# Kernel tuning notes

Measured on AMD Instinct MI355X. Metric: run time of the kernel, lower is better.

Reference implementation:

```python
import jax, jax.numpy as jnp
import numpy as np

NA, NT = 50000, 100000          # address / transaction node counts
FA, FT = 128, 64                # raw feature dims per node type
HID, OUT, HEADS, NCLS = 128, 64, 8, 2
E1, E2 = 500000, 250000         # cross-type / same-type edge counts
NEG_SLOPE = 0.2
LN_EPS = 1e-5


def _edge_att(xs, xd, src, dst, a_s, a_d, n_dst):
    # xs: [Ns,H,D] projected src feats, xd: [Nd,H,D] projected dst feats
    alpha_s = (xs * a_s).sum(-1)                     # [Ns,H]
    alpha_d = (xd * a_d).sum(-1)                     # [Nd,H]
    alpha = alpha_s[src] + alpha_d[dst]              # [E,H]
    alpha = jnp.where(alpha > 0, alpha, NEG_SLOPE * alpha)  # leaky_relu(0.2)
    # segment softmax over incoming edges of each dst node
    m = jax.lax.stop_gradient(jax.ops.segment_max(alpha, dst, num_segments=n_dst))
    m = jnp.where(jnp.isfinite(m), m, 0.0)
    ex = jnp.exp(alpha - m[dst])
    denom = jax.ops.segment_sum(ex, dst, num_segments=n_dst)
    w = ex / jnp.maximum(denom[dst], 1e-16)          # [E,H]
    msg = xs[src] * w[:, :, None]                    # [E,H,D]
    out = jax.ops.segment_sum(msg, dst, num_segments=n_dst)
    return jax.nn.relu(out.reshape(n_dst, -1))       # [Nd, H*D] (HANConv relu per edge type)


def _group(outs, q, kW, kb):
    # semantic-level attention over metapaths; outs: [K,N,F]
    score = (jnp.tanh(outs @ kW + kb).mean(axis=1) * q).sum(-1)  # [K]
    attn = jax.nn.softmax(score)
    return jnp.einsum('k,knf->nf', attn, outs)


def _layer_norm(x, g, b):
    mu = x.mean(-1, keepdims=True)
    var = ((x - mu) ** 2).mean(-1, keepdims=True)
    return (x - mu) / jnp.sqrt(var + LN_EPS) * g + b


def _han_conv(xa, xt, edges, Wa, ba, Wt, bt, atts, q, kW, kb):
    C = Wa.shape[1]
    D = C // HEADS
    za = (xa @ Wa + ba).reshape(-1, HEADS, D)
    zt = (xt @ Wt + bt).reshape(-1, HEADS, D)
    (eat_s, eat_d), (eta_s, eta_d), (eaa_s, eaa_d), (ett_s, ett_d) = edges
    (as_at, ad_at), (as_ta, ad_ta), (as_aa, ad_aa), (as_tt, ad_tt) = atts
    o_at = _edge_att(za, zt, eat_s, eat_d, as_at, ad_at, zt.shape[0])  # -> transaction
    o_ta = _edge_att(zt, za, eta_s, eta_d, as_ta, ad_ta, za.shape[0])  # -> address
    o_aa = _edge_att(za, za, eaa_s, eaa_d, as_aa, ad_aa, za.shape[0])  # -> address
    o_tt = _edge_att(zt, zt, ett_s, ett_d, as_tt, ad_tt, zt.shape[0])  # -> transaction
    new_a = _group(jnp.stack([o_ta, o_aa]), q, kW, kb)
    new_t = _group(jnp.stack([o_at, o_tt]), q, kW, kb)
    return new_a, new_t


def _forward(x_address, x_transaction,
             W_a1, b_a1, W_t1, b_t1,
             as_at1, ad_at1, as_ta1, ad_ta1, as_aa1, ad_aa1, as_tt1, ad_tt1,
             k1_W, k1_b, q1,
             W_a2, b_a2, W_t2, b_t2,
             as_at2, ad_at2, as_ta2, ad_ta2, as_aa2, ad_aa2, as_tt2, ad_tt2,
             k2_W, k2_b, q2,
             ln1_g, ln1_b, ln2_g, ln2_b, lin_W, lin_b, edges):
    atts1 = ((as_at1, ad_at1), (as_ta1, ad_ta1), (as_aa1, ad_aa1), (as_tt1, ad_tt1))
    atts2 = ((as_at2, ad_at2), (as_ta2, ad_ta2), (as_aa2, ad_aa2), (as_tt2, ad_tt2))
    xa, xt = _han_conv(x_address, x_transaction, edges, W_a1, b_a1, W_t1, b_t1, atts1, q1, k1_W, k1_b)
    xa = jax.nn.relu(_layer_norm(xa, ln1_g, ln1_b))
    xt = jax.nn.relu(_layer_norm(xt, ln1_g, ln1_b))
    # dropout is identity in eval mode
    xa, xt = _han_conv(xa, xt, edges, W_a2, b_a2, W_t2, b_t2, atts2, q2, k2_W, k2_b)
    xa = jax.nn.relu(_layer_norm(xa, ln2_g, ln2_b))
    return xa @ lin_W + lin_b                          # [NA, NCLS]


def setup_inputs() -> dict:
    key = jax.random.key(0)
    ks = jax.random.split(key, 40)
    D1, D2 = HID // HEADS, OUT // HEADS
    def n(i, shape, s=0.1):
        return jax.random.normal(ks[i], shape, jnp.float32) * s
    inp = {
        'x_address': jax.random.normal(ks[0], (NA, FA), jnp.float32),
        'x_transaction': jax.random.normal(ks[1], (NT, FT), jnp.float32),
        'eat_src': jax.random.randint(ks[2], (E1,), 0, NA),
        'eat_dst': jax.random.randint(ks[3], (E1,), 0, NT),
        'eta_src': jax.random.randint(ks[4], (E1,), 0, NT),
        'eta_dst': jax.random.randint(ks[5], (E1,), 0, NA),
        'eaa_src': jax.random.randint(ks[6], (E2,), 0, NA),
        'eaa_dst': jax.random.randint(ks[7], (E2,), 0, NA),
        'ett_src': jax.random.randint(ks[8], (E2,), 0, NT),
        'ett_dst': jax.random.randint(ks[9], (E2,), 0, NT),
        'W_a1': n(10, (FA, HID)), 'b_a1': jnp.zeros((HID,), jnp.float32),
        'W_t1': n(11, (FT, HID)), 'b_t1': jnp.zeros((HID,), jnp.float32),
        'as_at1': n(12, (HEADS, D1)), 'ad_at1': n(13, (HEADS, D1)),
        'as_ta1': n(14, (HEADS, D1)), 'ad_ta1': n(15, (HEADS, D1)),
        'as_aa1': n(16, (HEADS, D1)), 'ad_aa1': n(17, (HEADS, D1)),
        'as_tt1': n(18, (HEADS, D1)), 'ad_tt1': n(19, (HEADS, D1)),
        'k1_W': n(20, (HID, HID)), 'k1_b': jnp.zeros((HID,), jnp.float32), 'q1': n(21, (HID,)),
        'W_a2': n(22, (HID, OUT)), 'b_a2': jnp.zeros((OUT,), jnp.float32),
        'W_t2': n(23, (HID, OUT)), 'b_t2': jnp.zeros((OUT,), jnp.float32),
        'as_at2': n(24, (HEADS, D2)), 'ad_at2': n(25, (HEADS, D2)),
        'as_ta2': n(26, (HEADS, D2)), 'ad_ta2': n(27, (HEADS, D2)),
        'as_aa2': n(28, (HEADS, D2)), 'ad_aa2': n(29, (HEADS, D2)),
        'as_tt2': n(30, (HEADS, D2)), 'ad_tt2': n(31, (HEADS, D2)),
        'k2_W': n(32, (OUT, OUT)), 'k2_b': jnp.zeros((OUT,), jnp.float32), 'q2': n(33, (OUT,)),
        'ln1_g': jnp.ones((HID,), jnp.float32), 'ln1_b': jnp.zeros((HID,), jnp.float32),
        'ln2_g': jnp.ones((OUT,), jnp.float32), 'ln2_b': jnp.zeros((OUT,), jnp.float32),
        'lin_W': n(34, (OUT, NCLS)), 'lin_b': jnp.zeros((NCLS,), jnp.float32),
    }
    return inp


def reference(x_address, x_transaction,
              eat_src, eat_dst, eta_src, eta_dst, eaa_src, eaa_dst, ett_src, ett_dst,
              W_a1, b_a1, W_t1, b_t1,
              as_at1, ad_at1, as_ta1, ad_ta1, as_aa1, ad_aa1, as_tt1, ad_tt1,
              k1_W, k1_b, q1,
              W_a2, b_a2, W_t2, b_t2,
              as_at2, ad_at2, as_ta2, ad_ta2, as_aa2, ad_aa2, as_tt2, ad_tt2,
              k2_W, k2_b, q2,
              ln1_g, ln1_b, ln2_g, ln2_b, lin_W, lin_b):
    edges = ((eat_src, eat_dst), (eta_src, eta_dst), (eaa_src, eaa_dst), (ett_src, ett_dst))
    return _forward(x_address, x_transaction,
                    W_a1, b_a1, W_t1, b_t1,
                    as_at1, ad_at1, as_ta1, ad_ta1, as_aa1, ad_aa1, as_tt1, ad_tt1,
                    k1_W, k1_b, q1,
                    W_a2, b_a2, W_t2, b_t2,
                    as_at2, ad_at2, as_ta2, ad_ta2, as_aa2, ad_aa2, as_tt2, ad_tt2,
                    k2_W, k2_b, q2,
                    ln1_g, ln1_b, ln2_g, ln2_b, lin_W, lin_b, edges)
```

## Files before the change

### kernel.cpp

```cpp
#include <hip/hip_runtime.h>
#include <cstdint>
#include <cstddef>
#include <type_traits>

#define NA 50000
#define NT 100000
#define FA 128
#define FT 64
#define HID 128
#define OUTF 64
#define HEADS 8
#define E1 500000
#define E2 250000
#define NTOT (2*NT + 2*NA)
#define ETOT (2*E1 + 2*E2)
#define NSH 8

typedef __attribute__((ext_vector_type(8))) short short8;
typedef __attribute__((ext_vector_type(4))) float f32x4;

static __device__ __forceinline__ ushort f2b(float f) {
  unsigned int u = __float_as_uint(f);
  return (ushort)((u + 0x7fffu + ((u >> 16) & 1u)) >> 16);
}
static __device__ __forceinline__ float b2f(ushort b) {
  return __uint_as_float(((unsigned int)b) << 16);
}
static __device__ __forceinline__ float u2f_lo(unsigned int u) {
  return __uint_as_float(u << 16);
}
static __device__ __forceinline__ float u2f_hi(unsigned int u) {
  return __uint_as_float(u & 0xffff0000u);
}

template<int KK, typename AT>
__device__ __forceinline__ void gemm_fullk(
    const AT* __restrict__ A, const float* __restrict__ W,
    int N, int M, int row0, int col0,
    ushort* __restrict__ Als, ushort* __restrict__ Bls, f32x4* acc)
{
  constexpr int LP = KK + 8;
  int t = threadIdx.x;
  int w = t >> 6, lane = t & 63;
  int l15 = lane & 15, l4 = lane >> 4;
  {
    int arow = t >> 2, ac0 = (t & 3) * (KK / 4);
    bool aok = (row0 + arow) < N;
    const AT* Ap = A + (size_t)(row0 + arow) * KK + ac0;
#pragma unroll
    for (int j = 0; j < KK / 32; j++) {
      union { ushort u[8]; uint4 v; } pa;
      if (aok) {
        if constexpr (std::is_same<AT, float>::value) {
          float4 a0 = *reinterpret_cast<const float4*>(Ap + j*8);
          float4 a1 = *reinterpret_cast<const float4*>(Ap + j*8 + 4);
          pa.u[0]=f2b(a0.x); pa.u[1]=f2b(a0.y); pa.u[2]=f2b(a0.z); pa.u[3]=f2b(a0.w);
          pa.u[4]=f2b(a1.x); pa.u[5]=f2b(a1.y); pa.u[6]=f2b(a1.z); pa.u[7]=f2b(a1.w);
        } else {
          pa.v = *reinterpret_cast<const uint4*>(Ap + j*8);
        }
      } else {
        pa.v = make_uint4(0,0,0,0);
      }
      *reinterpret_cast<uint4*>(&Als[arow * LP + ac0 + j*8]) = pa.v;
    }
  }
  {
    int col = t & 63, kb = t >> 6;
    const float* Wp = W + (size_t)(col0 + col);
#pragma unroll
    for (int j = 0; j < KK / 32; j++) {
      int k0 = kb * (KK / 4) + j * 8;
      union { ushort u[8]; uint4 v; } pb;
#pragma unroll
      for (int i = 0; i < 8; i++)
        pb.u[i] = f2b(Wp[(size_t)(k0 + i) * M]);
      *reinterpret_cast<uint4*>(&Bls[col * LP + k0]) = pb.v;
    }
  }
  __syncthreads();
#pragma unroll
  for (int ks = 0; ks < KK / 32; ks++) {
    short8 af = *reinterpret_cast<const short8*>(
        &Als[(16*w + l15) * LP + ks*32 + l4*8]);
#pragma unroll
    for (int n = 0; n < 4; n++) {
      short8 bf = *reinterpret_cast<const short8*>(
          &Bls[(16*n + l15) * LP + ks*32 + l4*8]);
      acc[n] = __builtin_amdgcn_mfma_f32_16x16x32_bf16(af, bf, acc[n], 0, 0, 0);
    }
  }
}

template<int NV, int DD, int KK, typename AT>
__global__ __launch_bounds__(256) void zgemm_k(
    const AT* __restrict__ A, const float* __restrict__ W,
    const float* __restrict__ bias,
    const float* __restrict__ v0, const float* __restrict__ v1,
    const float* __restrict__ v2, const float* __restrict__ v3,
    float* __restrict__ o0, float* __restrict__ o1,
    float* __restrict__ o2, float* __restrict__ o3,
    ushort* __restrict__ Cb, int N, int M)
{
  __shared__ __align__(16) ushort Als[64 * (KK + 8)];
  __shared__ __align__(16) ushort Bls[64 * (KK + 8)];
  int t = threadIdx.x;
  int row0 = blockIdx.x * 64, col0 = blockIdx.y * 64;
  int w = t >> 6, lane = t & 63;
  int l15 = lane & 15, l4 = lane >> 4;
  f32x4 acc[4] = {{0.f,0.f,0.f,0.f},{0.f,0.f,0.f,0.f},
                  {0.f,0.f,0.f,0.f},{0.f,0.f,0.f,0.f}};
  gemm_fullk<KK, AT>(A, W, N, M, row0, col0, Als, Bls, acc);

  float vals[4][4];
#pragma unroll
  for (int n = 0; n < 4; n++) {
    int col = col0 + 16*n + l15;
    float bv = bias[col];
#pragma unroll
    for (int r = 0; r < 4; r++) {
      int row = row0 + 16*w + l4*4 + r;
      float v = acc[n][r] + bv;
      vals[n][r] = v;
      if (row < N) Cb[(size_t)row * M + col] = f2b(v);
    }
  }
#pragma unroll
  for (int n = 0; n < 4; n++) {
    int head = (DD == 16) ? (blockIdx.y*4 + n) : (n*2 + (l15 >> 3));
    int vi = head * DD + (l15 & (DD - 1));
    float w0 = v0[vi];
    float w1 = (NV > 1) ? v1[vi] : 0.f;
    float w2 = (NV > 2) ? v2[vi] : 0.f;
    float w3 = (NV > 3) ? v3[vi] : 0.f;
#pragma unroll
    for (int r = 0; r < 4; r++) {
      int row = row0 + 16*w + l4*4 + r;
      float zv = vals[n][r];
      float a0 = zv * w0, a1 = zv * w1, a2 = zv * w2, a3 = zv * w3;
#pragma unroll
      for (int o = 1; o < DD; o <<= 1) {
        a0 += __shfl_xor(a0, o);
        if (NV > 1) a1 += __shfl_xor(a1, o);
        if (NV > 2) a2 += __shfl_xor(a2, o);
        if (NV > 3) a3 += __shfl_xor(a3, o);
      }
      if ((l15 & (DD - 1)) == 0 && row < N) {
        o0[(size_t)row * 8 + head] = a0;
        if (NV > 1) o1[(size_t)row * 8 + head] = a1;
        if (NV > 2) o2[(size_t)row * 8 + head] = a2;
        if (NV > 3) o3[(size_t)row * 8 + head] = a3;
      }
    }
  }
}

template<int KK>
__global__ __launch_bounds__(256) void score_k(
    const ushort* __restrict__ A0, const ushort* __restrict__ A1,
    const ushort* __restrict__ A2, const ushort* __restrict__ A3,
    const float* __restrict__ W, const float* __restrict__ bias,
    const float* __restrict__ qv, float* __restrict__ scp,
    int4 cum, int4 Ns, int4 Gs, int M)
{
  __shared__ __align__(16) ushort Als[64 * (KK + 8)];
  __shared__ __align__(16) ushort Bls[64 * (KK + 8)];
  __shared__ float red[4];
  int b = blockIdx.x;
  int tsk, base, G, N; const ushort* A;
  if      (b < cum.x) { tsk=0; base=0;     G=Gs.x; N=Ns.x; A=A0; }
  else if (b < cum.y) { tsk=1; base=cum.x; G=Gs.y; N=Ns.y; A=A1; }
  else if (b < cum.z) { tsk=2; base=cum.y; G=Gs.z; N=Ns.z; A=A2; }
  else                { tsk=3; base=cum.z; G=Gs.w; N=Ns.w; A=A3; }
  int local = b - base;
  int row0 = (local % G) * 64, col0 = (local / G) * 64;
  int t = threadIdx.x;
  int w = t >> 6, lane = t & 63;
  int l15 = lane & 15, l4 = lane >> 4;
  f32x4 acc[4] = {{0.f,0.f,0.f,0.f},{0.f,0.f,0.f,0.f},
                  {0.f,0.f,0.f,0.f},{0.f,0.f,0.f,0.f}};
  gemm_fullk<KK, ushort>(A, W, N, M, row0, col0, Als, Bls, acc);

  float local_s = 0.f;
#pragma unroll
  for (int n = 0; n < 4; n++) {
    int col = col0 + 16*n + l15;
    float bv = bias[col], qq = qv[col];
#pragma unroll
    for (int r = 0; r < 4; r++) {
      int row = row0 + 16*w + l4*4 + r;
      if (row < N) local_s += tanhf(acc[n][r] + bv) * qq;
    }
  }
#pragma unroll
  for (int o = 32; o > 0; o >>= 1) local_s += __shfl_xor(local_s, o);
  if (lane == 0) red[w] = local_s;
  __syncthreads();
  if (t == 0) atomicAdd(&scp[tsk], red[0] + red[1] + red[2] + red[3]);
}

__global__ void hist4_sh(const int* __restrict__ d0, const int* __restrict__ d1,
    const int* __restrict__ d2, const int* __restrict__ d3,
    int* __restrict__ cnt8, float* __restrict__ scp)
{
  if (blockIdx.x == 0 && threadIdx.x < 8) scp[threadIdx.x] = 0.f;
  int e = blockIdx.x * 256 + threadIdx.x;
  int sh = blockIdx.x & (NSH - 1);
  int d;
  if      (e < E1)          d = d0[e];
  else if (e < 2*E1)        d = d1[e - E1] + NT;
  else if (e < 2*E1 + E2)   d = d2[e - 2*E1] + NT + NA;
  else if (e < ETOT)        d = d3[e - 2*E1 - E2] + NT + 2*NA;
  else return;
  atomicAdd(&cnt8[sh * NTOT + d], 1);
}

__global__ void scatter_sh(const int* __restrict__ s0, const int* __restrict__ d0,
    const int* __restrict__ s1, const int* __restrict__ d1,
    const int* __restrict__ s2, const int* __restrict__ d2,
    const int* __restrict__ s3, const int* __restrict__ d3,
    int* __restrict__ cur8, int* __restrict__ ssh)
{
  int e = blockIdx.x * 256 + threadIdx.x;
  int sh = blockIdx.x & (NSH - 1);
  int d, s;
  if      (e < E1)          { d = d0[e];                           s = s0[e]; }
  else if (e < 2*E1)        { d = d1[e - E1] + NT;                 s = s1[e - E1]; }
  else if (e < 2*E1 + E2)   { d = d2[e - 2*E1] + NT + NA;          s = s2[e - 2*E1]; }
  else if (e < ETOT)        { d = d3[e - 2*E1 - E2] + NT + 2*NA;   s = s3[e - 2*E1 - E2]; }
  else return;
  int p = atomicAdd(&cur8[sh * NTOT + d], 1);
  ssh[p] = s;
}

__global__ void sumsh_k(const int* __restrict__ cnt8, int* __restrict__ cnt)
{
  int g = blockIdx.x * 256 + threadIdx.x;
  if (g >= NTOT) return;
  int s = 0;
#pragma unroll
  for (int k = 0; k < NSH; k++) s += cnt8[k * NTOT + g];
  cnt[g] = s;
}

__global__ void compact_k(const int* __restrict__ rp8, const int* __restrict__ rp,
    const int* __restrict__ ssh, int* __restrict__ ssrc)
{
  int g = blockIdx.x * 256 + threadIdx.x;
  if (g >= NTOT) return;
  int w = rp[g];
#pragma unroll
  for (int s = 0; s < NSH; s++) {
    int b0 = rp8[s * NTOT + g], b1 = rp8[s * NTOT + g + 1];
    for (int e = b0; e < b1; e++) ssrc[w++] = ssh[e];
  }
}

__global__ __launch_bounds__(256) void scan_blk(const int* __restrict__ in,
    int* __restrict__ rp1, int* __restrict__ bsum, int n)
{
  __shared__ int sh[256];
  int base = blockIdx.x * 2048;
  int t = threadIdx.x;
  int v[8]; int s = 0;
#pragma unroll
  for (int k = 0; k < 8; k++) {
    int i = base + t * 8 + k;
    v[k] = (i < n) ? in[i] : 0; s += v[k];
  }
  sh[t] = s; __syncthreads();
  for (int o = 1; o < 256; o <<= 1) {
    int x = (t >= o) ? sh[t - o] : 0;
    __syncthreads(); sh[t] += x; __syncthreads();
  }
  int run = (t == 0) ? 0 : sh[t - 1];
  if (t == 255 && bsum) bsum[blockIdx.x] = sh[255];
#pragma unroll
  for (int k = 0; k < 8; k++) {
    int i = base + t * 8 + k;
    run += v[k];
    if (i < n) rp1[i] = run;
  }
}

__global__ void scan_add2(int* __restrict__ rp, int* __restrict__ cur,
    const int* __restrict__ bsA, int n)
{
  int i = blockIdx.x * blockDim.x + threadIdx.x;
  if (i == 0) { rp[0] = 0; cur[0] = 0; }
  if (i < n) {
    int blk = i >> 11;
    int base = blk ? bsA[blk - 1] : 0;
    int v = rp[i + 1] + base;
    rp[i + 1] = v;
    if (i + 1 < n) cur[i + 1] = v;
  }
}

__global__ void scan_add(int* __restrict__ rp, const int* __restrict__ bsA, int n)
{
  int i = blockIdx.x * blockDim.x + threadIdx.x;
  if (i == 0) rp[0] = 0;
  if (i < n) {
    int blk = i >> 11;
    int base = blk ? bsA[blk - 1] : 0;
    rp[i + 1] += base;
  }
}

struct AggTask {
  int g0, Nd;
  const float* als; const float* ald;
  const ushort* z;  ushort* out;
};

template<int F>
__global__ __launch_bounds__(256) void agg_multi(const int* __restrict__ rp,
    const int* __restrict__ ssrc, AggTask T0, AggTask T1, AggTask T2, AggTask T3,
    int c1, int c2, int c3)
{
  constexpr int LPN = (F == 128) ? 16 : 8;
  constexpr int NPW = 64 / LPN;
  int b = blockIdx.x;
  AggTask T; int lb;
  if      (b < c1) { T = T0; lb = b; }
  else if (b < c2) { T = T1; lb = b - c1; }
  else if (b < c3) { T = T2; lb = b - c2; }
  else             { T = T3; lb = b - c3; }
  int wv = threadIdx.x >> 6, lane = threadIdx.x & 63;
  int grp = lane / LPN, lg = lane % LPN;
  int n = (lb * 4 + wv) * NPW + grp;
  if (n >= T.Nd) return;
  int g = T.g0 + n;
  int start = rp[g], end = rp[g + 1];
  int hh = (F == 128) ? (lg >> 1) : lg;
  float ad_h = T.ald[(size_t)n * 8 + hh];

  float den = 0.f;
  float acc[8] = {};
  for (int e = start; e < end; e++) {
    int sn = ssrc[e];
    uint4 zv = *reinterpret_cast<const uint4*>(T.z + (size_t)sn * F + lg * 8);
    float a = T.als[(size_t)sn * 8 + hh] + ad_h;
    a = a > 0.f ? a : 0.2f * a;
    float p = __expf(fminf(a, 30.f));
    den += p;
    acc[0] = fmaf(p, u2f_lo(zv.x), acc[0]);
    acc[1] = fmaf(p, u2f_hi(zv.x), acc[1]);
    acc[2] = fmaf(p, u2f_lo(zv.y), acc[2]);
    acc[3] = fmaf(p, u2f_hi(zv.y), acc[3]);
    acc[4] = fmaf(p, u2f_lo(zv.z), acc[4]);
    acc[5] = fmaf(p, u2f_hi(zv.z), acc[5]);
    acc[6] = fmaf(p, u2f_lo(zv.w), acc[6]);
    acc[7] = fmaf(p, u2f_hi(zv.w), acc[7]);
  }
  float inv = 1.f / fmaxf(den, 1e-16f);
  unsigned int pk[4];
#pragma unroll
  for (int k2 = 0; k2 < 4; k2++)
    pk[k2] = (unsigned int)f2b(fmaxf(acc[2*k2] * inv, 0.f))
           | ((unsigned int)f2b(fmaxf(acc[2*k2+1] * inv, 0.f)) << 16);
  *reinterpret_cast<uint4*>(T.out + (size_t)n * F + lg * 8)
      = make_uint4(pk[0], pk[1], pk[2], pk[3]);
}

__global__ __launch_bounds__(256) void combine2_k(
    const ushort* __restrict__ o00, const ushort* __restrict__ o01,
    const float* __restrict__ sc0, float invn0, ushort* __restrict__ out0, int N0,
    const ushort* __restrict__ o10, const ushort* __restrict__ o11,
    const float* __restrict__ sc1, float invn1, ushort* __restrict__ out1, int N1,
    const float* __restrict__ g, const float* __restrict__ bb)
{
  int c1 = (N0 + 3) / 4;
  int b = blockIdx.x;
  const ushort *o0, *o1; const float* sc; float invn; ushort* outp; int N, lb;
  if (b < c1) { o0=o00; o1=o01; sc=sc0; invn=invn0; outp=out0; N=N0; lb=b; }
  else        { o0=o10; o1=o11; sc=sc1; invn=invn1; outp=out1; N=N1; lb=b-c1; }
  int wv = threadIdx.x >> 6, lane = threadIdx.x & 63;
  int n = lb * 4 + wv;
  if (n >= N) return;
  float s0 = sc[0] * invn, s1 = sc[1] * invn;
  float mx = fmaxf(s0, s1);
  float e0 = __expf(s0 - mx), e1 = __expf(s1 - mx);
  float w0 = e0 / (e0 + e1), w1 = e1 / (e0 + e1);
  float x[2];
#pragma unroll
  for (int jj = 0; jj < 2; jj++) {
    int idx = lane + 64 * jj;
    x[jj] = w0 * b2f(o0[(size_t)n * 128 + idx]) + w1 * b2f(o1[(size_t)n * 128 + idx]);
  }
  float sum = x[0] + x[1];
#pragma unroll
  for (int o = 32; o > 0; o >>= 1) sum += __shfl_xor(sum, o);
  float mu = sum / 128.f;
  float vs = 0.f;
#pragma unroll
  for (int jj = 0; jj < 2; jj++) { float dd = x[jj] - mu; vs = fmaf(dd, dd, vs); }
#pragma unroll
  for (int o = 32; o > 0; o >>= 1) vs += __shfl_xor(vs, o);
  float rstd = rsqrtf(vs / 128.f + 1e-5f);
#pragma unroll
  for (int jj = 0; jj < 2; jj++) {
    int idx = lane + 64 * jj;
    float y = (x[jj] - mu) * rstd * g[idx] + bb[idx];
    outp[(size_t)n * 128 + idx] = f2b(fmaxf(y, 0.f));
  }
}

__global__ __launch_bounds__(256) void combine_final_k(
    const ushort* __restrict__ o0, const ushort* __restrict__ o1,
    const float* __restrict__ sc, float invn,
    const float* __restrict__ g, const float* __restrict__ bb,
    const float* __restrict__ lw, const float* __restrict__ lb,
    float* __restrict__ outp, int N)
{
  int wv = threadIdx.x >> 6, lane = threadIdx.x & 63;
  int n = blockIdx.x * 4 + wv;
  if (n >= N) return;
  float s0 = sc[0] * invn, s1 = sc[1] * invn;
  float mx = fmaxf(s0, s1);
  float e0 = __expf(s0 - mx), e1 = __expf(s1 - mx);
  float w0 = e0 / (e0 + e1), w1 = e1 / (e0 + e1);
  float x = w0 * b2f(o0[(size_t)n * 64 + lane]) + w1 * b2f(o1[(size_t)n * 64 + lane]);
  float sum = x;
#pragma unroll
  for (int o = 32; o > 0; o >>= 1) sum += __shfl_xor(sum, o);
  float mu = sum / 64.f;
  float dd = x - mu;
  float vs = dd * dd;
#pragma unroll
  for (int o = 32; o > 0; o >>= 1) vs += __shfl_xor(vs, o);
  float rstd = rsqrtf(vs / 64.f + 1e-5f);
  float y = fmaxf((x - mu) * rstd * g[lane] + bb[lane], 0.f);
  float p0 = y * lw[lane * 2 + 0];
  float p1 = y * lw[lane * 2 + 1];
#pragma unroll
  for (int o = 32; o > 0; o >>= 1) { p0 += __shfl_xor(p0, o); p1 += __shfl_xor(p1, o); }
  if (lane == 0) {
    outp[(size_t)n * 2 + 0] = p0 + lb[0];
    outp[(size_t)n * 2 + 1] = p1 + lb[1];
  }
}

extern "C" void kernel_launch(void* const* d_in, const int* in_sizes, int n_in,
                              void* d_out, int out_size, void* d_ws, size_t ws_size,
                              hipStream_t stream)
{
  (void)in_sizes; (void)n_in; (void)out_size;
  const float* x_a = (const float*)d_in[0];
  const float* x_t = (const float*)d_in[1];
  const int* eat_s = (const int*)d_in[2];
  const int* eat_d = (const int*)d_in[3];
  const int* eta_s = (const int*)d_in[4];
  const int* eta_d = (const int*)d_in[5];
  const int* eaa_s = (const int*)d_in[6];
  const int* eaa_d = (const int*)d_in[7];
  const int* ett_s = (const int*)d_in[8];
  const int* ett_d = (const int*)d_in[9];
  const float* W_a1 = (const float*)d_in[10]; const float* b_a1 = (const float*)d_in[11];
  const float* W_t1 = (const float*)d_in[12]; const float* b_t1 = (const float*)d_in[13];
  const float* as_at1 = (const float*)d_in[14]; const float* ad_at1 = (const float*)d_in[15];
  const float* as_ta1 = (const float*)d_in[16]; const float* ad_ta1 = (const float*)d_in[17];
  const float* as_aa1 = (const float*)d_in[18]; const float* ad_aa1 = (const float*)d_in[19];
  const float* as_tt1 = (const float*)d_in[20]; const float* ad_tt1 = (const float*)d_in[21];
  const float* k1_W = (const float*)d_in[22]; const float* k1_b = (const float*)d_in[23];
  const float* q1   = (const float*)d_in[24];
  const float* W_a2 = (const float*)d_in[25]; const float* b_a2 = (const float*)d_in[26];
  const float* W_t2 = (const float*)d_in[27]; const float* b_t2 = (const float*)d_in[28];
  const float* as_ta2 = (const float*)d_in[31]; const float* ad_ta2 = (const float*)d_in[32];
  const float* as_aa2 = (const float*)d_in[33]; const float* ad_aa2 = (const float*)d_in[34];
  const float* k2_W = (const float*)d_in[37]; const float* k2_b = (const float*)d_in[38];
  const float* q2   = (const float*)d_in[39];
  const float* ln1_g = (const float*)d_in[40]; const float* ln1_b = (const float*)d_in[41];
  const float* ln2_g = (const float*)d_in[42]; const float* ln2_b = (const float*)d_in[43];
  const float* lin_W = (const float*)d_in[44]; const float* lin_b = (const float*)d_in[45];

  char* ws = (char*)d_ws;
  size_t off = 0;
  auto alloc = [&](size_t bytes) {
    size_t o = off; off += (bytes + 255) & ~(size_t)255; return o;
  };
  size_t ZA1 = alloc((size_t)NA * HID * 2);
  size_t ZT1 = alloc((size_t)NT * HID * 2);
  size_t OTA = alloc((size_t)NA * HID * 2);
  size_t OAA = alloc((size_t)NA * HID * 2);
  size_t OAT = alloc((size_t)NT * HID * 2);
  size_t OTT = alloc((size_t)NT * HID * 2);
  size_t A_AS_AT = alloc((size_t)NA * 8 * 4);
  size_t A_AD_TA = alloc((size_t)NA * 8 * 4);
  size_t A_AS_AA = alloc((size_t)NA * 8 * 4);
  size_t A_AD_AA = alloc((size_t)NA * 8 * 4);
  size_t A_T_D_AT = alloc((size_t)NT * 8 * 4);
  size_t A_T_S_TA = alloc((size_t)NT * 8 * 4);
  size_t A_T_S_TT = alloc((size_t)NT * 8 * 4);
  size_t A_T_D_TT = alloc((size_t)NT * 8 * 4);
  size_t RP8  = alloc(((size_t)NSH * NTOT + 1) * 4);
  size_t CUR8 = alloc((size_t)NSH * NTOT * 4);
  size_t SSH  = alloc((size_t)ETOT * 4);
  size_t RP   = alloc((size_t)(NTOT + 1) * 4);
  size_t CNT  = alloc((size_t)NTOT * 4);
  size_t SS   = alloc((size_t)ETOT * 4);
  size_t BSM  = alloc(2048 * 4);
  size_t BSM2 = alloc(256 * 4);
  size_t SC   = alloc(256);
  if (off > ws_size) return;

  ushort* za1 = (ushort*)(ws + ZA1);
  ushort* zt1 = (ushort*)(ws + ZT1);
  ushort* ota = (ushort*)(ws + OTA);
  ushort* oaa = (ushort*)(ws + OAA);
  ushort* oat = (ushort*)(ws + OAT);
  ushort* ott = (ushort*)(ws + OTT);
  float* aASAT = (float*)(ws + A_AS_AT);
  float* aADTA = (float*)(ws + A_AD_TA);
  float* aASAA = (float*)(ws + A_AS_AA);
  float* aADAA = (float*)(ws + A_AD_AA);
  float* aTDAT = (float*)(ws + A_T_D_AT);
  float* aTSTA = (float*)(ws + A_T_S_TA);
  float* aTSTT = (float*)(ws + A_T_S_TT);
  float* aTDTT = (float*)(ws + A_T_D_TT);
  int* rp8  = (int*)(ws + RP8);
  int* cur8 = (int*)(ws + CUR8);
  int* ssh  = (int*)(ws + SSH);
  int* rp   = (int*)(ws + RP);
  int* cnt  = (int*)(ws + CNT);
  int* ssrc = (int*)(ws + SS);
  int* bsum = (int*)(ws + BSM);
  int* bsum2= (int*)(ws + BSM2);
  float* scp = (float*)(ws + SC);
  ushort* za2 = za1;
  ushort* zt2 = zt1;
  ushort* ota2 = oaa;
  ushort* oaa2 = (ushort*)(ws + OAA + (size_t)NA * OUTF * 2);

  const int GA = (NA + 63) / 64, GT = (NT + 63) / 64;
  const int EBL = (ETOT + 255) / 256;
  const int SCN8 = NSH * NTOT;
  const int SBL8 = (SCN8 + 2047) / 2048;
  const int SBL1 = (NTOT + 2047) / 2048;

  hipMemsetAsync(cur8, 0, (size_t)SCN8 * 4, stream);
  hist4_sh<<<EBL, 256, 0, stream>>>(eat_d, eta_d, eaa_d, ett_d, cur8, scp);
  sumsh_k<<<(NTOT + 255) / 256, 256, 0, stream>>>(cur8, cnt);
  scan_blk<<<SBL8, 256, 0, stream>>>(cur8, rp8 + 1, bsum, SCN8);
  scan_blk<<<1, 256, 0, stream>>>(bsum, bsum, nullptr, SBL8);
  scan_add2<<<(SCN8 + 255) / 256, 256, 0, stream>>>(rp8, cur8, bsum, SCN8);
  scan_blk<<<SBL1, 256, 0, stream>>>(cnt, rp + 1, bsum2, NTOT);
  scan_blk<<<1, 256, 0, stream>>>(bsum2, bsum2, nullptr, SBL1);
  scan_add<<<(NTOT + 255) / 256, 256, 0, stream>>>(rp, bsum2, NTOT);
  scatter_sh<<<EBL, 256, 0, stream>>>(eat_s, eat_d, eta_s, eta_d,
                                      eaa_s, eaa_d, ett_s, ett_d, cur8, ssh);
  compact_k<<<(NTOT + 255) / 256, 256, 0, stream>>>(rp8, rp, ssh, ssrc);

  zgemm_k<4,16,FA,float><<<dim3(GA,2),256,0,stream>>>(x_a, W_a1, b_a1,
      as_at1, ad_ta1, as_aa1, ad_aa1, aASAT, aADTA, aASAA, aADAA,
      za1, NA, HID);
  zgemm_k<4,16,FT,float><<<dim3(GT,2),256,0,stream>>>(x_t, W_t1, b_t1,
      ad_at1, as_ta1, as_tt1, ad_tt1, aTDAT, aTSTA, aTSTT, aTDTT,
      zt1, NT, HID);
  {
    const int BT = (NT + 15) / 16, BA = (NA + 15) / 16;
    AggTask T0{0,          NT, aASAT, aTDAT, za1, oat};
    AggTask T1{NT,         NA, aTSTA, aADTA, zt1, ota};
    AggTask T2{NT+NA,      NA, aASAA, aADAA, za1, oaa};
    AggTask T3{NT+2*NA,    NT, aTSTT, aTDTT, zt1, ott};
    agg_multi<128><<<2*BT + 2*BA, 256, 0, stream>>>(rp, ssrc,
        T0, T1, T2, T3, BT, BT + BA, BT + 2*BA);
  }
  score_k<HID><<<4*GA + 4*GT, 256, 0, stream>>>(ota, oaa, oat, ott,
      k1_W, k1_b, q1, scp,
      make_int4(2*GA, 4*GA, 4*GA + 2*GT, 4*GA + 4*GT),
      make_int4(NA, NA, NT, NT), make_int4(GA, GA, GT, GT), HID);
  combine2_k<<<(NA/4) + (NT/4), 256, 0, stream>>>(
      ota, oaa, scp + 0, 1.f/NA, ota, NA,
      oat, ott, scp + 2, 1.f/NT, oat, NT, ln1_g, ln1_b);

  zgemm_k<3,8,HID,ushort><<<dim3(GA,1),256,0,stream>>>(ota, W_a2, b_a2,
      ad_ta2, as_aa2, ad_aa2, nullptr, aADTA, aASAA, aADAA, nullptr,
      za2, NA, OUTF);
  zgemm_k<1,8,HID,ushort><<<dim3(GT,1),256,0,stream>>>(oat, W_t2, b_t2,
      as_ta2, nullptr, nullptr, nullptr, aTSTA, nullptr, nullptr, nullptr,
      zt2, NT, OUTF);
  {
    const int BA2 = (NA + 31) / 32;
    AggTask T0{NT,    NA, aTSTA, aADTA, zt2, ota2};
    AggTask T1{NT+NA, NA, aASAA, aADAA, za2, oaa2};
    agg_multi<64><<<2*BA2, 256, 0, stream>>>(rp, ssrc,
        T0, T1, T1, T1, BA2, 2*BA2, 2*BA2);
  }
  score_k<OUTF><<<2*GA, 256, 0, stream>>>(ota2, oaa2, ota2, ota2,
      k2_W, k2_b, q2, scp + 4,
      make_int4(GA, 2*GA, 2*GA, 2*GA),
      make_int4(NA, NA, NA, NA), make_int4(GA, GA, GA, GA), OUTF);
  combine_final_k<<<NA/4, 256, 0, stream>>>(ota2, oaa2, scp + 4, 1.f/NA,
      ln2_g, ln2_b, lin_W, lin_b, (float*)d_out, NA);
}
```

Measured before the change: 600.7 us.

## Make GEMM blocks persistent over row tiles with full-width staged weights

The projection and semantic-score GEMM kernels now stage the whole weight matrix (all output columns) in LDS once per block. Each block loops over several 64-row tiles and prefetches the next A tile into registers while the current tile runs its MFMAs. The LDS layout switches from padded rows to an XOR swizzle to avoid bank conflicts. This removes the repeated fp32-to-bf16 weight conversion per tile and the column-split grid that re-read A, at the cost of fewer blocks, more LDS per block and higher register pressure.

```diff
diff --git a/kernel.cpp b/kernel.cpp
--- a/kernel.cpp
+++ b/kernel.cpp
@@ -33,66 +33,107 @@
   return __uint_as_float(u & 0xffff0000u);
 }
 
+template<int KK>
+static __device__ __forceinline__ int lidx(int row, int off) {
+  return row * KK + (off ^ ((row & 7) << 3));
+}
+
+template<int KK, int M>
+static __device__ __forceinline__ void stageB(const float* __restrict__ W,
+                                              ushort* __restrict__ Bls)
+{
+  constexpr int TPC = 256 / M;
+  constexpr int CH  = KK / TPC;
+  constexpr int BL  = (CH < 16) ? CH : 16;
+  int t = threadIdx.x;
+  int col = t % M;
+  int k0 = (t / M) * CH;
+  const float* Wp = W + col;
+#pragma unroll
+  for (int b = 0; b < CH; b += BL) {
+    float v[BL];
+#pragma unroll
+    for (int i = 0; i < BL; i++) v[i] = Wp[(size_t)(k0 + b + i) * M];
+#pragma unroll
+    for (int q = 0; q < BL / 8; q++) {
+      union { ushort u[8]; uint4 x; } p;
+#pragma unroll
+      for (int i = 0; i < 8; i++) p.u[i] = f2b(v[q * 8 + i]);
+      *reinterpret_cast<uint4*>(&Bls[lidx<KK>(col, k0 + b + q * 8)]) = p.x;
+    }
+  }
+}
+
 template<int KK, typename AT>
-__device__ __forceinline__ void gemm_fullk(
-    const AT* __restrict__ A, const float* __restrict__ W,
-    int N, int M, int row0, int col0,
-    ushort* __restrict__ Als, ushort* __restrict__ Bls, f32x4* acc)
-{
-  constexpr int LP = KK + 8;
+struct ARegs {
+  float4 f[std::is_same<AT, float>::value ? KK / 16 : 1];
+  uint4  u[std::is_same<AT, float>::value ? 1 : KK / 32];
+};
+
+template<int KK, typename AT>
+static __device__ __forceinline__ void loadA(const AT* __restrict__ A, int N,
+                                             int row0, ARegs<KK, AT>& R)
+{
   int t = threadIdx.x;
-  int w = t >> 6, lane = t & 63;
+  int arow = t >> 2, ac0 = (t & 3) * (KK / 4);
+  int row = row0 + arow;
+  bool ok = row < N;
+  const AT* Ap = A + (size_t)row * KK + ac0;
+  if constexpr (std::is_same<AT, float>::value) {
+#pragma unroll
+    for (int j = 0; j < KK / 16; j++)
+      R.f[j] = ok ? *reinterpret_cast<const float4*>(Ap + j * 4)
+                  : make_float4(0.f, 0.f, 0.f, 0.f);
+  } else {
+#pragma unroll
+    for (int j = 0; j < KK / 32; j++)
+      R.u[j] = ok ? *reinterpret_cast<const uint4*>(Ap + j * 8)
+                  : make_uint4(0, 0, 0, 0);
+  }
+}
+
+template<int KK, typename AT>
+static __device__ __forceinline__ void writeA(const ARegs<KK, AT>& R,
+                                              ushort* __restrict__ Als)
+{
+  int t = threadIdx.x;
+  int arow = t >> 2, ac0 = (t & 3) * (KK / 4);
+#pragma unroll
+  for (int j = 0; j < KK / 32; j++) {
+    uint4 w;
+    if constexpr (std::is_same<AT, float>::value) {
+      union { ushort u[8]; uint4 x; } p;
+      float4 a0 = R.f[2 * j], a1 = R.f[2 * j + 1];
+      p.u[0] = f2b(a0.x); p.u[1] = f2b(a0.y); p.u[2] = f2b(a0.z); p.u[3] = f2b(a0.w);
+      p.u[4] = f2b(a1.x); p.u[5] = f2b(a1.y); p.u[6] = f2b(a1.z); p.u[7] = f2b(a1.w);
+      w = p.x;
+    } else {
+      w = R.u[j];
+    }
+    *reinterpret_cast<uint4*>(&Als[lidx<KK>(arow, ac0 + j * 8)]) = w;
+  }
+}
+
+template<int KK, int NCT>
+static __device__ __forceinline__ void mfma_tile(const ushort* __restrict__ Als,
+    const ushort* __restrict__ Bls, f32x4* acc)
+{
+  int lane = threadIdx.x & 63, w = threadIdx.x >> 6;
   int l15 = lane & 15, l4 = lane >> 4;
-  {
-    int arow = t >> 2, ac0 = (t & 3) * (KK / 4);
-    bool aok = (row0 + arow) < N;
-    const AT* Ap = A + (size_t)(row0 + arow) * KK + ac0;
-#pragma unroll
-    for (int j = 0; j < KK / 32; j++) {
-      union { ushort u[8]; uint4 v; } pa;
-      if (aok) {
-        if constexpr (std::is_same<AT, float>::value) {
-          float4 a0 = *reinterpret_cast<const float4*>(Ap + j*8);
-          float4 a1 = *reinterpret_cast<const float4*>(Ap + j*8 + 4);
-          pa.u[0]=f2b(a0.x); pa.u[1]=f2b(a0.y); pa.u[2]=f2b(a0.z); pa.u[3]=f2b(a0.w);
-          pa.u[4]=f2b(a1.x); pa.u[5]=f2b(a1.y); pa.u[6]=f2b(a1.z); pa.u[7]=f2b(a1.w);
-        } else {
-          pa.v = *reinterpret_cast<const uint4*>(Ap + j*8);
-        }
-      } else {
-        pa.v = make_uint4(0,0,0,0);
-      }
-      *reinterpret_cast<uint4*>(&Als[arow * LP + ac0 + j*8]) = pa.v;
-    }
-  }
-  {
-    int col = t & 63, kb = t >> 6;
-    const float* Wp = W + (size_t)(col0 + col);
-#pragma unroll
-    for (int j = 0; j < KK / 32; j++) {
-      int k0 = kb * (KK / 4) + j * 8;
-      union { ushort u[8]; uint4 v; } pb;
-#pragma unroll
-      for (int i = 0; i < 8; i++)
-        pb.u[i] = f2b(Wp[(size_t)(k0 + i) * M]);
-      *reinterpret_cast<uint4*>(&Bls[col * LP + k0]) = pb.v;
-    }
-  }
-  __syncthreads();
 #pragma unroll
   for (int ks = 0; ks < KK / 32; ks++) {
     short8 af = *reinterpret_cast<const short8*>(
-        &Als[(16*w + l15) * LP + ks*32 + l4*8]);
-#pragma unroll
-    for (int n = 0; n < 4; n++) {
+        &Als[lidx<KK>(16 * w + l15, ks * 32 + l4 * 8)]);
+#pragma unroll
+    for (int n = 0; n < NCT; n++) {
       short8 bf = *reinterpret_cast<const short8*>(
-          &Bls[(16*n + l15) * LP + ks*32 + l4*8]);
+          &Bls[lidx<KK>(16 * n + l15, ks * 32 + l4 * 8)]);
       acc[n] = __builtin_amdgcn_mfma_f32_16x16x32_bf16(af, bf, acc[n], 0, 0, 0);
     }
   }
 }
 
-template<int NV, int DD, int KK, typename AT>
+template<int NV, int DD, int KK, int M, int TPB, typename AT>
 __global__ __launch_bounds__(256) void zgemm_k(
     const AT* __restrict__ A, const float* __restrict__ W,
     const float* __restrict__ bias,
@@ -100,101 +141,131 @@
     const float* __restrict__ v2, const float* __restrict__ v3,
     float* __restrict__ o0, float* __restrict__ o1,
     float* __restrict__ o2, float* __restrict__ o3,
-    ushort* __restrict__ Cb, int N, int M)
-{
-  __shared__ __align__(16) ushort Als[64 * (KK + 8)];
-  __shared__ __align__(16) ushort Bls[64 * (KK + 8)];
-  int t = threadIdx.x;
-  int row0 = blockIdx.x * 64, col0 = blockIdx.y * 64;
-  int w = t >> 6, lane = t & 63;
+    ushort* __restrict__ Cb, int N)
+{
+  constexpr int NCT = M / 16;
+  __shared__ __align__(16) ushort Bls[M * KK];
+  __shared__ __align__(16) ushort Als[64 * KK];
+  int t = threadIdx.x, w = t >> 6, lane = t & 63;
   int l15 = lane & 15, l4 = lane >> 4;
-  f32x4 acc[4] = {{0.f,0.f,0.f,0.f},{0.f,0.f,0.f,0.f},
-                  {0.f,0.f,0.f,0.f},{0.f,0.f,0.f,0.f}};
-  gemm_fullk<KK, AT>(A, W, N, M, row0, col0, Als, Bls, acc);
-
-  float vals[4][4];
-#pragma unroll
-  for (int n = 0; n < 4; n++) {
-    int col = col0 + 16*n + l15;
-    float bv = bias[col];
-#pragma unroll
-    for (int r = 0; r < 4; r++) {
-      int row = row0 + 16*w + l4*4 + r;
-      float v = acc[n][r] + bv;
-      vals[n][r] = v;
-      if (row < N) Cb[(size_t)row * M + col] = f2b(v);
-    }
-  }
-#pragma unroll
-  for (int n = 0; n < 4; n++) {
-    int head = (DD == 16) ? (blockIdx.y*4 + n) : (n*2 + (l15 >> 3));
+  int ntiles = (N + 63) >> 6;
+  int tile0 = blockIdx.x * TPB;
+  int nt = min(TPB, ntiles - tile0);
+
+  stageB<KK, M>(W, Bls);
+  ARegs<KK, AT> R;
+  loadA<KK, AT>(A, N, tile0 * 64, R);
+
+  float bv[NCT], aw0[NCT], aw1[NCT], aw2[NCT], aw3[NCT];
+#pragma unroll
+  for (int n = 0; n < NCT; n++) {
+    int col = 16 * n + l15;
+    bv[n] = bias[col];
+    int head = (DD == 16) ? n : (n * 2 + (l15 >> 3));
     int vi = head * DD + (l15 & (DD - 1));
-    float w0 = v0[vi];
-    float w1 = (NV > 1) ? v1[vi] : 0.f;
-    float w2 = (NV > 2) ? v2[vi] : 0.f;
-    float w3 = (NV > 3) ? v3[vi] : 0.f;
-#pragma unroll
-    for (int r = 0; r < 4; r++) {
-      int row = row0 + 16*w + l4*4 + r;
-      float zv = vals[n][r];
-      float a0 = zv * w0, a1 = zv * w1, a2 = zv * w2, a3 = zv * w3;
-#pragma unroll
-      for (int o = 1; o < DD; o <<= 1) {
-        a0 += __shfl_xor(a0, o);
-        if (NV > 1) a1 += __shfl_xor(a1, o);
-        if (NV > 2) a2 += __shfl_xor(a2, o);
-        if (NV > 3) a3 += __shfl_xor(a3, o);
-      }
-      if ((l15 & (DD - 1)) == 0 && row < N) {
-        o0[(size_t)row * 8 + head] = a0;
-        if (NV > 1) o1[(size_t)row * 8 + head] = a1;
-        if (NV > 2) o2[(size_t)row * 8 + head] = a2;
-        if (NV > 3) o3[(size_t)row * 8 + head] = a3;
+    aw0[n] = v0[vi];
+    aw1[n] = (NV > 1) ? v1[vi] : 0.f;
+    aw2[n] = (NV > 2) ? v2[vi] : 0.f;
+    aw3[n] = (NV > 3) ? v3[vi] : 0.f;
+  }
+
+  for (int i = 0; i < nt; i++) {
+    int row0 = (tile0 + i) * 64;
+    __syncthreads();
+    writeA<KK, AT>(R, Als);
+    __syncthreads();
+    if (i + 1 < nt) loadA<KK, AT>(A, N, row0 + 64, R);
+    f32x4 acc[NCT];
+#pragma unroll
+    for (int n = 0; n < NCT; n++) acc[n] = (f32x4){0.f, 0.f, 0.f, 0.f};
+    mfma_tile<KK, NCT>(Als, Bls, acc);
+
+#pragma unroll
+    for (int n = 0; n < NCT; n++) {
+      int col = 16 * n + l15;
+      int head = (DD == 16) ? n : (n * 2 + (l15 >> 3));
+#pragma unroll
+      for (int r = 0; r < 4; r++) {
+        int row = row0 + 16 * w + l4 * 4 + r;
+        float v = acc[n][r] + bv[n];
+        if (row < N) Cb[(size_t)row * M + col] = f2b(v);
+        float a0 = v * aw0[n], a1 = v * aw1[n], a2 = v * aw2[n], a3 = v * aw3[n];
+#pragma unroll
+        for (int o = 1; o < DD; o <<= 1) {
+          a0 += __shfl_xor(a0, o);
+          if (NV > 1) a1 += __shfl_xor(a1, o);
+          if (NV > 2) a2 += __shfl_xor(a2, o);
+          if (NV > 3) a3 += __shfl_xor(a3, o);
+        }
+        if ((l15 & (DD - 1)) == 0 && row < N) {
+          o0[(size_t)row * 8 + head] = a0;
+          if (NV > 1) o1[(size_t)row * 8 + head] = a1;
+          if (NV > 2) o2[(size_t)row * 8 + head] = a2;
+          if (NV > 3) o3[(size_t)row * 8 + head] = a3;
+        }
       }
     }
   }
 }
 
-template<int KK>
+template<int KK, int M, int TPB>
 __global__ __launch_bounds__(256) void score_k(
     const ushort* __restrict__ A0, const ushort* __restrict__ A1,
     const ushort* __restrict__ A2, const ushort* __restrict__ A3,
     const float* __restrict__ W, const float* __restrict__ bias,
     const float* __restrict__ qv, float* __restrict__ scp,
-    int4 cum, int4 Ns, int4 Gs, int M)
-{
-  __shared__ __align__(16) ushort Als[64 * (KK + 8)];
-  __shared__ __align__(16) ushort Bls[64 * (KK + 8)];
+    int4 cumB, int4 Ns)
+{
+  constexpr int NCT = M / 16;
+  __shared__ __align__(16) ushort Bls[M * KK];
+  __shared__ __align__(16) ushort Als[64 * KK];
   __shared__ float red[4];
   int b = blockIdx.x;
-  int tsk, base, G, N; const ushort* A;
-  if      (b < cum.x) { tsk=0; base=0;     G=Gs.x; N=Ns.x; A=A0; }
-  else if (b < cum.y) { tsk=1; base=cum.x; G=Gs.y; N=Ns.y; A=A1; }
-  else if (b < cum.z) { tsk=2; base=cum.y; G=Gs.z; N=Ns.z; A=A2; }
-  else                { tsk=3; base=cum.z; G=Gs.w; N=Ns.w; A=A3; }
-  int local = b - base;
-  int row0 = (local % G) * 64, col0 = (local / G) * 64;
-  int t = threadIdx.x;
-  int w = t >> 6, lane = t & 63;
+  int tsk, bbase, N; const ushort* A;
+  if      (b < cumB.x) { tsk = 0; bbase = 0;      N = Ns.x; A = A0; }
+  else if (b < cumB.y) { tsk = 1; bbase = cumB.x; N = Ns.y; A = A1; }
+  else if (b < cumB.z) { tsk = 2; bbase = cumB.y; N = Ns.z; A = A2; }
+  else                 { tsk = 3; bbase = cumB.z; N = Ns.w; A = A3; }
+  int t = threadIdx.x, w = t >> 6, lane = t & 63;
   int l15 = lane & 15, l4 = lane >> 4;
-  f32x4 acc[4] = {{0.f,0.f,0.f,0.f},{0.f,0.f,0.f,0.f},
-                  {0.f,0.f,0.f,0.f},{0.f,0.f,0.f,0.f}};
-  gemm_fullk<KK, ushort>(A, W, N, M, row0, col0, Als, Bls, acc);
-
-  float local_s = 0.f;
-#pragma unroll
-  for (int n = 0; n < 4; n++) {
-    int col = col0 + 16*n + l15;
-    float bv = bias[col], qq = qv[col];
-#pragma unroll
-    for (int r = 0; r < 4; r++) {
-      int row = row0 + 16*w + l4*4 + r;
-      if (row < N) local_s += tanhf(acc[n][r] + bv) * qq;
+  int ntiles = (N + 63) >> 6;
+  int tile0 = (b - bbase) * TPB;
+  int nt = min(TPB, ntiles - tile0);
+
+  stageB<KK, M>(W, Bls);
+  ARegs<KK, ushort> R;
+  loadA<KK, ushort>(A, N, tile0 * 64, R);
+
+  float bb[NCT], qb[NCT];
+#pragma unroll
+  for (int n = 0; n < NCT; n++) {
+    int col = 16 * n + l15;
+    bb[n] = bias[col]; qb[n] = qv[col];
+  }
+
+  float ls = 0.f;
+  for (int i = 0; i < nt; i++) {
+    int row0 = (tile0 + i) * 64;
+    __syncthreads();
+    writeA<KK, ushort>(R, Als);
+    __syncthreads();
+    if (i + 1 < nt) loadA<KK, ushort>(A, N, row0 + 64, R);
+    f32x4 acc[NCT];
+#pragma unroll
+    for (int n = 0; n < NCT; n++) acc[n] = (f32x4){0.f, 0.f, 0.f, 0.f};
+    mfma_tile<KK, NCT>(Als, Bls, acc);
+#pragma unroll
+    for (int n = 0; n < NCT; n++) {
+#pragma unroll
+      for (int r = 0; r < 4; r++) {
+        int row = row0 + 16 * w + l4 * 4 + r;
+        if (row < N) ls += tanhf(acc[n][r] + bb[n]) * qb[n];
+      }
     }
   }
 #pragma unroll
-  for (int o = 32; o > 0; o >>= 1) local_s += __shfl_xor(local_s, o);
-  if (lane == 0) red[w] = local_s;
+  for (int o = 32; o > 0; o >>= 1) ls += __shfl_xor(ls, o);
+  if (lane == 0) red[w] = ls;
   __syncthreads();
   if (t == 0) atomicAdd(&scp[tsk], red[0] + red[1] + red[2] + red[3]);
 }
@@ -533,7 +604,7 @@
   ushort* ota2 = oaa;
   ushort* oaa2 = (ushort*)(ws + OAA + (size_t)NA * OUTF * 2);
 
-  const int GA = (NA + 63) / 64, GT = (NT + 63) / 64;
+  const int TA = (NA + 63) / 64, TT = (NT + 63) / 64;
   const int EBL = (ETOT + 255) / 256;
   const int SCN8 = NSH * NTOT;
   const int SBL8 = (SCN8 + 2047) / 2048;
@@ -552,12 +623,10 @@
                                       eaa_s, eaa_d, ett_s, ett_d, cur8, ssh);
   compact_k<<<(NTOT + 255) / 256, 256, 0, stream>>>(rp8, rp, ssh, ssrc);
 
-  zgemm_k<4,16,FA,float><<<dim3(GA,2),256,0,stream>>>(x_a, W_a1, b_a1,
-      as_at1, ad_ta1, as_aa1, ad_aa1, aASAT, aADTA, aASAA, aADAA,
-      za1, NA, HID);
-  zgemm_k<4,16,FT,float><<<dim3(GT,2),256,0,stream>>>(x_t, W_t1, b_t1,
-      ad_at1, as_ta1, as_tt1, ad_tt1, aTDAT, aTSTA, aTSTT, aTDTT,
-      zt1, NT, HID);
+  zgemm_k<4,16,FA,HID,2,float><<<(TA+1)/2,256,0,stream>>>(x_a, W_a1, b_a1,
+      as_at1, ad_ta1, as_aa1, ad_aa1, aASAT, aADTA, aASAA, aADAA, za1, NA);
+  zgemm_k<4,16,FT,HID,4,float><<<(TT+3)/4,256,0,stream>>>(x_t, W_t1, b_t1,
+      ad_at1, as_ta1, as_tt1, ad_tt1, aTDAT, aTSTA, aTSTT, aTDTT, zt1, NT);
   {
     const int BT = (NT + 15) / 16, BA = (NA + 15) / 16;
     AggTask T0{0,          NT, aASAT, aTDAT, za1, oat};
@@ -567,20 +636,21 @@
     agg_multi<128><<<2*BT + 2*BA, 256, 0, stream>>>(rp, ssrc,
         T0, T1, T2, T3, BT, BT + BA, BT + 2*BA);
   }
-  score_k<HID><<<4*GA + 4*GT, 256, 0, stream>>>(ota, oaa, oat, ott,
-      k1_W, k1_b, q1, scp,
-      make_int4(2*GA, 4*GA, 4*GA + 2*GT, 4*GA + 4*GT),
-      make_int4(NA, NA, NT, NT), make_int4(GA, GA, GT, GT), HID);
+  {
+    const int bA = (TA + 3) / 4, bT = (TT + 3) / 4;
+    score_k<HID,HID,4><<<2*bA + 2*bT, 256, 0, stream>>>(ota, oaa, oat, ott,
+        k1_W, k1_b, q1, scp,
+        make_int4(bA, 2*bA, 2*bA + bT, 2*bA + 2*bT),
+        make_int4(NA, NA, NT, NT));
+  }
   combine2_k<<<(NA/4) + (NT/4), 256, 0, stream>>>(
       ota, oaa, scp + 0, 1.f/NA, ota, NA,
       oat, ott, scp + 2, 1.f/NT, oat, NT, ln1_g, ln1_b);
 
-  zgemm_k<3,8,HID,ushort><<<dim3(GA,1),256,0,stream>>>(ota, W_a2, b_a2,
-      ad_ta2, as_aa2, ad_aa2, nullptr, aADTA, aASAA, aADAA, nullptr,
-      za2, NA, OUTF);
-  zgemm_k<1,8,HID,ushort><<<dim3(GT,1),256,0,stream>>>(oat, W_t2, b_t2,
-      as_ta2, nullptr, nullptr, nullptr, aTSTA, nullptr, nullptr, nullptr,
-      zt2, NT, OUTF);
+  zgemm_k<3,8,HID,OUTF,2,ushort><<<(TA+1)/2,256,0,stream>>>(ota, W_a2, b_a2,
+      ad_ta2, as_aa2, ad_aa2, nullptr, aADTA, aASAA, aADAA, nullptr, za2, NA);
+  zgemm_k<1,8,HID,OUTF,4,ushort><<<(TT+3)/4,256,0,stream>>>(oat, W_t2, b_t2,
+      as_ta2, nullptr, nullptr, nullptr, aTSTA, nullptr, nullptr, nullptr, zt2, NT);
   {
     const int BA2 = (NA + 31) / 32;
     AggTask T0{NT,    NA, aTSTA, aADTA, zt2, ota2};
@@ -588,10 +658,13 @@
     agg_multi<64><<<2*BA2, 256, 0, stream>>>(rp, ssrc,
         T0, T1, T1, T1, BA2, 2*BA2, 2*BA2);
   }
-  score_k<OUTF><<<2*GA, 256, 0, stream>>>(ota2, oaa2, ota2, ota2,
-      k2_W, k2_b, q2, scp + 4,
-      make_int4(GA, 2*GA, 2*GA, 2*GA),
-      make_int4(NA, NA, NA, NA), make_int4(GA, GA, GA, GA), OUTF);
+  {
+    const int bA = (TA + 3) / 4;
+    score_k<OUTF,OUTF,4><<<2*bA, 256, 0, stream>>>(ota2, oaa2, ota2, ota2,
+        k2_W, k2_b, q2, scp + 4,
+        make_int4(bA, 2*bA, 2*bA, 2*bA),
+        make_int4(NA, NA, NA, NA));
+  }
   combine_final_k<<<NA/4, 256, 0, stream>>>(ota2, oaa2, scp + 4, 1.f/NA,
       ln2_g, ln2_b, lin_W, lin_b, (float*)d_out, NA);
 }
```

New measurement: 518.4 us. 13.7% less time.
